# Kernel tuning notes

Measured on AMD Instinct MI355X. Metric: run time of the kernel, lower is better.

The kernel has to match this reference:

```python
import jax, jax.numpy as jnp
import numpy as np
import math

EPS = 1e-12
SQRT_2_OVER_PI = math.sqrt(2.0 / math.pi)

B, S, H = 8, 2048, 4096


def setup_inputs() -> dict:
    key = jax.random.key(0)
    k1, k2 = jax.random.split(key)
    x = jax.random.normal(k1, (B, S, H), dtype=jnp.float32)
    # Linear weight in torch layout [out, in]; scaled like nn.Linear default init
    W = jax.random.normal(k2, (H, H), dtype=jnp.float32) * (1.0 / math.sqrt(H))
    b = jnp.zeros((H,), dtype=jnp.float32)
    a2 = jnp.ones((H,), dtype=jnp.float32)   # LayerNorm scale
    b2 = jnp.zeros((H,), dtype=jnp.float32)  # LayerNorm shift
    return {"x": x, "W": W, "b": b, "a2": a2, "b2": b2}


def gelu_tanh(h):
    return 0.5 * h * (1.0 + jnp.tanh(SQRT_2_OVER_PI * (h + 0.044715 * h * h * h)))


def reference(x, W, b, a2, b2):
    # Linear: x @ W^T + b  (torch nn.Linear convention)
    h = jnp.einsum("bsh,oh->bso", x, W) + b
    g = gelu_tanh(h)
    # Custom LayerNorm (biased var, eps=1e-12): g*inv + (b2 - mean*inv)
    mean = jnp.mean(g, axis=-1, keepdims=True)
    var = jnp.mean(jnp.square(g - mean), axis=-1, keepdims=True)
    inv = jax.lax.rsqrt(var + EPS) * a2
    return g * inv + (b2 - mean * inv)
```

## Files before the change

kernel.cpp:

```cpp
#include <hip/hip_runtime.h>
#include <hip/hip_bf16.h>
#include <stdint.h>

#define M_TOTAL 16384
#define K_DIM   4096
#define N_DIM   4096
#define BM 128
#define BN 128
#define BK 32
#define NK (K_DIM / BK)

typedef unsigned short u16;
typedef __attribute__((ext_vector_type(4))) float  f32x4;
typedef __attribute__((ext_vector_type(8))) short  bf16x8;
typedef __attribute__((ext_vector_type(8))) unsigned short u16x8;

__device__ __forceinline__ u16 f2bf_rn(float f) {
    union { float f; uint32_t u; } x; x.f = f;
    uint32_t r = x.u + 0x7FFFu + ((x.u >> 16) & 1u);
    return (u16)(r >> 16);
}
__device__ __forceinline__ float bf2f(u16 s) {
    union { uint32_t u; float f; } x; x.u = ((uint32_t)s) << 16;
    return x.f;
}

#define ASYNC16(gp, lp) \
    __builtin_amdgcn_global_load_lds((const __attribute__((address_space(1))) void*)(gp), \
                                     (__attribute__((address_space(3))) void*)(lp), 16, 0, 0)

__global__ __launch_bounds__(256) void split_kernel(const float* __restrict__ in,
                                                    u16* __restrict__ hi,
                                                    u16* __restrict__ lo,
                                                    int nvec) {
    int i = blockIdx.x * 256 + threadIdx.x;
    if (i >= nvec) return;
    f32x4 v0 = ((const f32x4*)in)[2*i];
    f32x4 v1 = ((const f32x4*)in)[2*i + 1];
    u16x8 hv, lv;
#pragma unroll
    for (int j = 0; j < 8; ++j) {
        float f = (j < 4) ? v0[j] : v1[j - 4];
        u16 h = f2bf_rn(f);
        hv[j] = h;
        lv[j] = f2bf_rn(f - bf2f(h));
    }
    ((u16x8*)hi)[i] = hv;
    ((u16x8*)lo)[i] = lv;
}

__global__ __launch_bounds__(256, 2)
void gemm_gelu_kernel(const u16* __restrict__ xh, const u16* __restrict__ xl,
                      const u16* __restrict__ wh, const u16* __restrict__ wl,
                      const float* __restrict__ bias, float* __restrict__ out) {
    __shared__ __align__(16) u16 sAh[BM * BK];
    __shared__ __align__(16) u16 sAl[BM * BK];
    __shared__ __align__(16) u16 sBh[BN * BK];
    __shared__ __align__(16) u16 sBl[BN * BK];

    const int tid  = threadIdx.x;
    const int lane = tid & 63;
    const int wid  = tid >> 6;

    const int nwg = gridDim.x;
    const int cpx = nwg >> 3;
    const int swz = (blockIdx.x & 7) * cpx + (blockIdx.x >> 3);
    const int bm = swz >> 5;
    const int bn = swz & 31;

    const int row0 = bm * BM;
    const int col0 = bn * BN;

    const int c0 = tid;
    const int c1 = 256 + tid;
    const size_t aOff0 = (size_t)(row0 + (c0 >> 2)) * K_DIM + ((c0 & 3) << 3);
    const size_t aOff1 = (size_t)(row0 + (c1 >> 2)) * K_DIM + ((c1 & 3) << 3);
    const size_t bOff0 = (size_t)(col0 + (c0 >> 2)) * K_DIM + ((c0 & 3) << 3);
    const size_t bOff1 = (size_t)(col0 + (c1 >> 2)) * K_DIM + ((c1 & 3) << 3);

    f32x4 acc[4][4] = {};
    const int wrow = (wid >> 1) << 6;
    const int wcol = (wid & 1) << 6;
    const int fr = lane & 15;
    const int kq = (lane >> 4) << 3;

    for (int kt = 0; kt < NK; ++kt) {
        const size_t kofs = (size_t)kt * BK;
        ASYNC16(xh + aOff0 + kofs, sAh + c0 * 8);
        ASYNC16(xh + aOff1 + kofs, sAh + c1 * 8);
        ASYNC16(xl + aOff0 + kofs, sAl + c0 * 8);
        ASYNC16(xl + aOff1 + kofs, sAl + c1 * 8);
        ASYNC16(wh + bOff0 + kofs, sBh + c0 * 8);
        ASYNC16(wh + bOff1 + kofs, sBh + c1 * 8);
        ASYNC16(wl + bOff0 + kofs, sBl + c0 * 8);
        ASYNC16(wl + bOff1 + kofs, sBl + c1 * 8);
        __syncthreads();

        bf16x8 bh[4], bl[4];
#pragma unroll
        for (int n = 0; n < 4; ++n) {
            const int r = wcol + n * 16 + fr;
            bh[n] = *(const bf16x8*)(sBh + r * BK + kq);
            bl[n] = *(const bf16x8*)(sBl + r * BK + kq);
        }
#pragma unroll
        for (int m = 0; m < 4; ++m) {
            const int r = wrow + m * 16 + fr;
            bf16x8 ah = *(const bf16x8*)(sAh + r * BK + kq);
            bf16x8 al = *(const bf16x8*)(sAl + r * BK + kq);
#pragma unroll
            for (int n = 0; n < 4; ++n) {
                acc[m][n] = __builtin_amdgcn_mfma_f32_16x16x32_bf16(al, bh[n], acc[m][n], 0, 0, 0);
                acc[m][n] = __builtin_amdgcn_mfma_f32_16x16x32_bf16(ah, bl[n], acc[m][n], 0, 0, 0);
                acc[m][n] = __builtin_amdgcn_mfma_f32_16x16x32_bf16(ah, bh[n], acc[m][n], 0, 0, 0);
            }
        }
        __syncthreads();
    }

    const float SC = 0.7978845608028654f;
#pragma unroll
    for (int n = 0; n < 4; ++n) {
        const int col = col0 + wcol + n * 16 + (lane & 15);
        const float bc = bias[col];
#pragma unroll
        for (int m = 0; m < 4; ++m) {
            const int rbase = row0 + wrow + m * 16 + ((lane >> 4) << 2);
#pragma unroll
            for (int r = 0; r < 4; ++r) {
                float h = acc[m][n][r] + bc;
                float t = tanhf(SC * (h + 0.044715f * h * h * h));
                out[(size_t)(rbase + r) * N_DIM + col] = 0.5f * h * (1.0f + t);
            }
        }
    }
}

__global__ __launch_bounds__(256)
void ln_kernel(float* __restrict__ out, const float* __restrict__ a2,
               const float* __restrict__ b2) {
    const int row = blockIdx.x;
    float* g = out + (size_t)row * N_DIM;
    const int tid = threadIdx.x;

    f32x4 v[4];
    float s = 0.f;
#pragma unroll
    for (int j = 0; j < 4; ++j) {
        v[j] = ((const f32x4*)g)[j * 256 + tid];
        s += v[j][0] + v[j][1] + v[j][2] + v[j][3];
    }
#pragma unroll
    for (int o = 32; o > 0; o >>= 1) s += __shfl_xor(s, o, 64);
    __shared__ float red[4];
    if ((tid & 63) == 0) red[tid >> 6] = s;
    __syncthreads();
    s = red[0] + red[1] + red[2] + red[3];
    const float mean = s * (1.0f / N_DIM);

    float q = 0.f;
#pragma unroll
    for (int j = 0; j < 4; ++j)
#pragma unroll
        for (int e = 0; e < 4; ++e) { float d = v[j][e] - mean; q += d * d; }
#pragma unroll
    for (int o = 32; o > 0; o >>= 1) q += __shfl_xor(q, o, 64);
    __shared__ float red2[4];
    if ((tid & 63) == 0) red2[tid >> 6] = q;
    __syncthreads();
    q = red2[0] + red2[1] + red2[2] + red2[3];
    const float var = q * (1.0f / N_DIM);
    const float inv = 1.0f / sqrtf(var + 1e-12f);

#pragma unroll
    for (int j = 0; j < 4; ++j) {
        f32x4 av = ((const f32x4*)a2)[j * 256 + tid];
        f32x4 bv = ((const f32x4*)b2)[j * 256 + tid];
        f32x4 o4;
#pragma unroll
        for (int e = 0; e < 4; ++e) o4[e] = (v[j][e] - mean) * inv * av[e] + bv[e];
        ((f32x4*)g)[j * 256 + tid] = o4;
    }
}

extern "C" void kernel_launch(void* const* d_in, const int* in_sizes, int n_in,
                              void* d_out, int out_size, void* d_ws, size_t ws_size,
                              hipStream_t stream) {
    const float* x  = (const float*)d_in[0];
    const float* W  = (const float*)d_in[1];
    const float* b  = (const float*)d_in[2];
    const float* a2 = (const float*)d_in[3];
    const float* b2 = (const float*)d_in[4];
    float* out = (float*)d_out;

    char* ws = (char*)d_ws;
    u16* xh = (u16*)(ws);
    u16* xl = (u16*)(ws + 134217728ull);
    u16* wh = (u16*)(ws + 268435456ull);
    u16* wl = (u16*)(ws + 301989888ull);

    split_kernel<<<8388608 / 256, 256, 0, stream>>>(x, xh, xl, 8388608);
    split_kernel<<<2097152 / 256, 256, 0, stream>>>(W, wh, wl, 2097152);

    gemm_gelu_kernel<<<4096, 256, 0, stream>>>(xh, xl, wh, wl, b, out);

    ln_kernel<<<M_TOTAL, 256, 0, stream>>>(out, a2, b2);
}
```

Baseline: 2.663 ms.

## Double-buffer LDS tiles with next-tile prefetch and remap blocks per XCD

Allocates two LDS buffers for each of the hi/lo A and B tiles and issues the async loads for the next K tile before computing on the current one, to overlap global memory latency with MFMA work. It also changes the block-to-tile mapping so each XCD handles a fixed group of four column tiles, improving L2 reuse of weight tiles. LDS usage doubles, which may limit occupancy, and the barrier placement may still force waits on in-flight prefetches.

```diff
diff --git a/kernel.cpp b/kernel.cpp
--- a/kernel.cpp
+++ b/kernel.cpp
@@ -53,20 +53,22 @@
 void gemm_gelu_kernel(const u16* __restrict__ xh, const u16* __restrict__ xl,
                       const u16* __restrict__ wh, const u16* __restrict__ wl,
                       const float* __restrict__ bias, float* __restrict__ out) {
-    __shared__ __align__(16) u16 sAh[BM * BK];
-    __shared__ __align__(16) u16 sAl[BM * BK];
-    __shared__ __align__(16) u16 sBh[BN * BK];
-    __shared__ __align__(16) u16 sBl[BN * BK];
+    __shared__ __align__(16) u16 sAh[2][BM * BK];
+    __shared__ __align__(16) u16 sAl[2][BM * BK];
+    __shared__ __align__(16) u16 sBh[2][BN * BK];
+    __shared__ __align__(16) u16 sBl[2][BN * BK];
 
     const int tid  = threadIdx.x;
     const int lane = tid & 63;
     const int wid  = tid >> 6;
 
-    const int nwg = gridDim.x;
-    const int cpx = nwg >> 3;
-    const int swz = (blockIdx.x & 7) * cpx + (blockIdx.x >> 3);
-    const int bm = swz >> 5;
-    const int bn = swz & 31;
+    const int bid = blockIdx.x;
+    const int c  = bid & 7;
+    const int i  = bid >> 3;
+    const int r  = i >> 8;
+    const int j  = i & 255;
+    const int bm = j >> 1;
+    const int bn = (c << 2) + (r << 1) + (j & 1);
 
     const int row0 = bm * BM;
     const int col0 = bn * BN;
@@ -78,36 +80,43 @@
     const size_t bOff0 = (size_t)(col0 + (c0 >> 2)) * K_DIM + ((c0 & 3) << 3);
     const size_t bOff1 = (size_t)(col0 + (c1 >> 2)) * K_DIM + ((c1 & 3) << 3);
 
+    auto STAGE = [&](int buf, int kt) {
+        const size_t kofs = (size_t)kt * BK;
+        ASYNC16(xh + aOff0 + kofs, sAh[buf] + c0 * 8);
+        ASYNC16(xh + aOff1 + kofs, sAh[buf] + c1 * 8);
+        ASYNC16(xl + aOff0 + kofs, sAl[buf] + c0 * 8);
+        ASYNC16(xl + aOff1 + kofs, sAl[buf] + c1 * 8);
+        ASYNC16(wh + bOff0 + kofs, sBh[buf] + c0 * 8);
+        ASYNC16(wh + bOff1 + kofs, sBh[buf] + c1 * 8);
+        ASYNC16(wl + bOff0 + kofs, sBl[buf] + c0 * 8);
+        ASYNC16(wl + bOff1 + kofs, sBl[buf] + c1 * 8);
+    };
+
     f32x4 acc[4][4] = {};
     const int wrow = (wid >> 1) << 6;
     const int wcol = (wid & 1) << 6;
     const int fr = lane & 15;
     const int kq = (lane >> 4) << 3;
 
+    STAGE(0, 0);
+    __syncthreads();
+
     for (int kt = 0; kt < NK; ++kt) {
-        const size_t kofs = (size_t)kt * BK;
-        ASYNC16(xh + aOff0 + kofs, sAh + c0 * 8);
-        ASYNC16(xh + aOff1 + kofs, sAh + c1 * 8);
-        ASYNC16(xl + aOff0 + kofs, sAl + c0 * 8);
-        ASYNC16(xl + aOff1 + kofs, sAl + c1 * 8);
-        ASYNC16(wh + bOff0 + kofs, sBh + c0 * 8);
-        ASYNC16(wh + bOff1 + kofs, sBh + c1 * 8);
-        ASYNC16(wl + bOff0 + kofs, sBl + c0 * 8);
-        ASYNC16(wl + bOff1 + kofs, sBl + c1 * 8);
-        __syncthreads();
+        const int cur = kt & 1;
+        if (kt + 1 < NK) STAGE(cur ^ 1, kt + 1);
 
         bf16x8 bh[4], bl[4];
 #pragma unroll
         for (int n = 0; n < 4; ++n) {
-            const int r = wcol + n * 16 + fr;
-            bh[n] = *(const bf16x8*)(sBh + r * BK + kq);
-            bl[n] = *(const bf16x8*)(sBl + r * BK + kq);
+            const int rr = wcol + n * 16 + fr;
+            bh[n] = *(const bf16x8*)(sBh[cur] + rr * BK + kq);
+            bl[n] = *(const bf16x8*)(sBl[cur] + rr * BK + kq);
         }
 #pragma unroll
         for (int m = 0; m < 4; ++m) {
-            const int r = wrow + m * 16 + fr;
-            bf16x8 ah = *(const bf16x8*)(sAh + r * BK + kq);
-            bf16x8 al = *(const bf16x8*)(sAl + r * BK + kq);
+            const int rr = wrow + m * 16 + fr;
+            bf16x8 ah = *(const bf16x8*)(sAh[cur] + rr * BK + kq);
+            bf16x8 al = *(const bf16x8*)(sAl[cur] + rr * BK + kq);
 #pragma unroll
             for (int n = 0; n < 4; ++n) {
                 acc[m][n] = __builtin_amdgcn_mfma_f32_16x16x32_bf16(al, bh[n], acc[m][n], 0, 0, 0);
@@ -115,6 +124,7 @@
                 acc[m][n] = __builtin_amdgcn_mfma_f32_16x16x32_bf16(ah, bh[n], acc[m][n], 0, 0, 0);
             }
         }
+
         __syncthreads();
     }
 
@@ -127,10 +137,10 @@
         for (int m = 0; m < 4; ++m) {
             const int rbase = row0 + wrow + m * 16 + ((lane >> 4) << 2);
 #pragma unroll
-            for (int r = 0; r < 4; ++r) {
-                float h = acc[m][n][r] + bc;
+            for (int rr = 0; rr < 4; ++rr) {
+                float h = acc[m][n][rr] + bc;
                 float t = tanhf(SC * (h + 0.044715f * h * h * h));
-                out[(size_t)(rbase + r) * N_DIM + col] = 0.5f * h * (1.0f + t);
+                out[(size_t)(rbase + rr) * N_DIM + col] = 0.5f * h * (1.0f + t);
             }
         }
     }
```

Measured after the change: 2.412 ms. 1.1x faster.
